# Optimization experiments

Measured on AMD Instinct MI355X. Metric: run time of the kernel, lower is better.

The kernel has to match this reference:

```python
import jax, jax.numpy as jnp
import numpy as np

B, C_IN, C_OUT, K, H, W = 8, 512, 512, 3, 32, 32
EPS = 1e-8


def _fir_filter():
    f1 = jnp.array([1.0, 3.0, 3.0, 1.0], dtype=jnp.float32)
    f = jnp.outer(f1, f1)
    f = f / f.sum()
    return f * 4.0  # gain = 2**2, filter.ndim/2 == 1


def setup_inputs() -> dict:
    key = jax.random.key(0)
    k1, k2, k3 = jax.random.split(key, 3)
    x = jax.random.normal(k1, (B, C_IN, H, W), dtype=jnp.float32)
    styles = jax.random.normal(k2, (B, C_IN), dtype=jnp.float32)
    w = jax.random.normal(k3, (C_OUT, C_IN, K, K), dtype=jnp.float32)  # lr_multiplier=1
    return {"x": x, "styles": styles, "w": w}


def reference(x, styles, w):
    batch = x.shape[0]
    gain = 1.0 / np.sqrt(C_OUT * C_IN * K * K)
    # modulate: [B, O, I, kh, kw]
    wm = (w[None] * gain) * (styles[:, None, :, None, None] + 1.0)
    # demodulate
    dcoefs = jax.lax.rsqrt(jnp.sum(wm * wm, axis=(2, 3, 4)) + EPS)  # [B, O]
    wm = wm * dcoefs[:, :, None, None, None]
    # fused modconv: batch folded into channels/groups
    x1 = x.reshape(1, batch * C_IN, H, W)
    # torch conv_transpose2d(stride=2, padding=0, groups=B) == dilated conv with
    # spatially flipped kernel, lhs_dilation=2, padding=K-1 on each side.
    w_eq = jnp.flip(wm, axis=(-2, -1)).reshape(batch * C_OUT, C_IN, K, K)
    y = jax.lax.conv_general_dilated(
        x1, w_eq,
        window_strides=(1, 1),
        padding=[(K - 1, K - 1), (K - 1, K - 1)],
        lhs_dilation=(2, 2),
        feature_group_count=batch,
        dimension_numbers=("NCHW", "OIHW", "NCHW"),
    )  # [1, B*O, 2H+1, 2W+1]
    # Upfirdn2d: up=1, down=1, pad=[1,1,1,1], depthwise 4x4 FIR (cross-correlation;
    # filter is symmetric so no flip needed)
    C = batch * C_OUT
    f = jnp.broadcast_to(_fir_filter()[None, None], (C, 1, 4, 4))
    y = jax.lax.conv_general_dilated(
        y, f,
        window_strides=(1, 1),
        padding=[(1, 1), (1, 1)],
        feature_group_count=C,
        dimension_numbers=("NCHW", "OIHW", "NCHW"),
    )  # [1, B*O, 2H, 2W]
    return y.reshape(batch, C_OUT, 2 * H, 2 * W)
```

## Files before the change

### kernel.cpp

```cpp
#include <hip/hip_runtime.h>
#include <stdint.h>


#define DI __device__ __forceinline__

typedef __bf16 bf16x8 __attribute__((ext_vector_type(8)));
typedef float f32x4 __attribute__((ext_vector_type(4)));

DI float bf2f(ushort u) { union { uint32_t i; float f; } v; v.i = ((uint32_t)u) << 16; return v.f; }
DI ushort f2bf(float f) {
  union { float f; uint32_t i; } v; v.f = f;
  uint32_t x = v.i;
  return (ushort)((x + 0x7FFFu + ((x >> 16) & 1u)) >> 16);
}

#define GAIN (1.0f / 1536.0f)

__global__ __launch_bounds__(256) void k_prep(const float* __restrict__ w,
                                              const float* __restrict__ styles,
                                              const float* __restrict__ x,
                                              ushort* __restrict__ Wm,
                                              ushort* __restrict__ xt) {
  __shared__ union {
    struct { float ss[4096]; float dc[8]; float wred[4][8]; } wp;
    float tl[32][257];
  } sm;
  const int t = threadIdx.x;
  if (blockIdx.x < 512) {
    const int o = blockIdx.x;
#pragma unroll
    for (int j = 0; j < 4; j++) {
      const int idx = (t + j * 256) * 4;
      *(float4*)&sm.wp.ss[idx] = *(const float4*)&styles[idx];
    }
    float wreg[18];
    const float* wp_ = w + o * 4608 + t * 18;
#pragma unroll
    for (int k = 0; k < 9; k++) {
      float2 v2 = *(const float2*)(wp_ + 2 * k);
      wreg[2 * k] = v2.x;
      wreg[2 * k + 1] = v2.y;
    }
    float q0 = 0.f, q1 = 0.f;
#pragma unroll
    for (int k = 0; k < 9; k++) {
      q0 += wreg[k] * wreg[k];
      q1 += wreg[9 + k] * wreg[9 + k];
    }
    __syncthreads();
    float pb[8];
#pragma unroll
    for (int b = 0; b < 8; b++) {
      float s0 = sm.wp.ss[b * 512 + 2 * t] + 1.0f;
      float s1 = sm.wp.ss[b * 512 + 2 * t + 1] + 1.0f;
      pb[b] = s0 * s0 * q0 + s1 * s1 * q1;
    }
#pragma unroll
    for (int b = 0; b < 8; b++)
#pragma unroll
      for (int off = 32; off > 0; off >>= 1) pb[b] += __shfl_down(pb[b], off, 64);
    const int wid = t >> 6, lane = t & 63;
    if (lane == 0) {
#pragma unroll
      for (int b = 0; b < 8; b++) sm.wp.wred[wid][b] = pb[b];
    }
    __syncthreads();
    if (t < 8)
      sm.wp.dc[t] = rsqrtf((sm.wp.wred[0][t] + sm.wp.wred[1][t] + sm.wp.wred[2][t] + sm.wp.wred[3][t]) *
                               (GAIN * GAIN) + 1e-8f);
    __syncthreads();
#pragma unroll
    for (int b = 0; b < 8; b++) {
      const float d = sm.wp.dc[b];
      const float s0 = GAIN * (sm.wp.ss[b * 512 + 2 * t] + 1.0f) * d;
      const float s1 = GAIN * (sm.wp.ss[b * 512 + 2 * t + 1] + 1.0f) * d;
      ushort* base = Wm + ((size_t)(b * 9) * 512 + o) * 512 + 2 * t;
#pragma unroll
      for (int tap = 0; tap < 9; tap++) {
        ushort2 val = make_ushort2(f2bf(wreg[tap] * s0), f2bf(wreg[9 + tap] * s1));
        *(ushort2*)(base + (size_t)tap * 262144) = val;
      }
    }
  } else {
    const int idx = blockIdx.x - 512;
    const int hw0 = (idx & 3) * 256, i0 = ((idx >> 2) & 15) * 32, b = idx >> 6;
    const float* xb = x + b * (512 * 1024);
#pragma unroll
    for (int p = 0; p < 8; p++) {
      const int r = p * 4 + (t >> 6);
      const int c4 = (t & 63) * 4;
      float4 v = *(const float4*)&xb[(i0 + r) * 1024 + hw0 + c4];
      sm.tl[r][c4] = v.x; sm.tl[r][c4 + 1] = v.y; sm.tl[r][c4 + 2] = v.z; sm.tl[r][c4 + 3] = v.w;
    }
    __syncthreads();
    ushort* xtb = xt + b * (1024 * 512);
#pragma unroll
    for (int p = 0; p < 8; p++) {
      const int hw = p * 32 + (t >> 3);
      const int i4 = (t & 7) * 4;
      ushort4 v = make_ushort4(f2bf(sm.tl[i4][hw]), f2bf(sm.tl[i4 + 1][hw]),
                               f2bf(sm.tl[i4 + 2][hw]), f2bf(sm.tl[i4 + 3][hw]));
      *(ushort4*)&xtb[(hw0 + hw) * 512 + i0 + i4] = v;
    }
  }
}

__global__ __launch_bounds__(512, 2) void k_gemm(const ushort* __restrict__ A,
                                                 const ushort* __restrict__ Bt,
                                                 ushort* __restrict__ C) {
  __shared__ __attribute__((aligned(128))) char smem[114688];
  const int id = blockIdx.x;
  const int batch = id & 7;
  const int rem = id >> 3;
  const int mt = rem >> 2, nt = rem & 3;
  const int m0 = mt * 192, n0 = nt * 256;
  const ushort* Ag = A + (size_t)batch * (4608 * 512);
  const ushort* Bg = Bt + (size_t)batch * (1024 * 512);
  ushort* Cg = C + (size_t)batch * (4608 * 1024);

  const int tid = threadIdx.x;
  const int w = tid >> 6, lane = tid & 63;
  const int wm = w >> 2, wn = w & 3;
  const int lq = lane >> 4, l15 = lane & 15, l7 = lane & 7;
  const int rlow = lane >> 3;
  const int ssw = (lane & 7) ^ rlow;

  const char* pA = (const char*)Ag + (size_t)(m0 + w * 24 + rlow) * 1024 + ssw * 16;
  const char* pB = (const char*)Bg + (size_t)(n0 + w * 32 + rlow) * 1024 + ssw * 16;
  char* dA = smem + w * 3072;
  char* dB = smem + 49152 + w * 4096;

#define GLL(srcp, dstp)                                                                     \
  __builtin_amdgcn_global_load_lds((const __attribute__((address_space(1))) void*)(srcp),   \
                                   (__attribute__((address_space(3))) void*)(dstp), 16, 0, 0)
#define STAGE_A(buf, kt)                                            \
  do {                                                              \
    GLL(pA + 0 * 8192 + (kt) * 128, dA + (buf) * 24576 + 0 * 1024); \
    GLL(pA + 1 * 8192 + (kt) * 128, dA + (buf) * 24576 + 1 * 1024); \
    GLL(pA + 2 * 8192 + (kt) * 128, dA + (buf) * 24576 + 2 * 1024); \
  } while (0)
#define STAGE_B(buf, kt)                                            \
  do {                                                              \
    GLL(pB + 0 * 8192 + (kt) * 128, dB + (buf) * 32768 + 0 * 1024); \
    GLL(pB + 1 * 8192 + (kt) * 128, dB + (buf) * 32768 + 1 * 1024); \
    GLL(pB + 2 * 8192 + (kt) * 128, dB + (buf) * 32768 + 2 * 1024); \
    GLL(pB + 3 * 8192 + (kt) * 128, dB + (buf) * 32768 + 3 * 1024); \
  } while (0)
#define CF asm volatile("" ::: "memory")
#define BAR()                          \
  do {                                 \
    CF;                                \
    __builtin_amdgcn_s_barrier();      \
    CF;                                \
  } while (0)

  const char* Ard = smem + (wm * 96 + l15) * 128;
  const char* Brd = smem + 49152 + (wn * 64 + l15) * 128;
  const int s0o = (lq ^ l7) * 16;
  const int s1o = ((4 + lq) ^ l7) * 16;

  f32x4 acc[6][4];
  const f32x4 z4 = {0.f, 0.f, 0.f, 0.f};
#pragma unroll
  for (int i = 0; i < 6; ++i)
#pragma unroll
    for (int n = 0; n < 4; ++n) acc[i][n] = z4;

  STAGE_A(0, 0); STAGE_B(0, 0);
  STAGE_A(1, 1); STAGE_B(1, 1);
  asm volatile("s_waitcnt vmcnt(7)" ::: "memory");
  BAR();

#pragma unroll
  for (int t = 0; t < 8; ++t) {
    const int buf = t & 1;
    const char* Ab = Ard + buf * 24576;
    const char* Bb = Brd + buf * 32768;
    bf16x8 a[3][2], a2[3][2], b[4][2];
#pragma unroll
    for (int i = 0; i < 3; ++i) {
      a[i][0] = *(const bf16x8*)(Ab + i * 2048 + s0o);
      a[i][1] = *(const bf16x8*)(Ab + i * 2048 + s1o);
    }
#pragma unroll
    for (int n = 0; n < 2; ++n) {
      b[n][0] = *(const bf16x8*)(Bb + n * 2048 + s0o);
      b[n][1] = *(const bf16x8*)(Bb + n * 2048 + s1o);
    }
    BAR();
    __builtin_amdgcn_s_setprio(1);
#pragma unroll
    for (int kk = 0; kk < 2; ++kk)
#pragma unroll
      for (int n = 0; n < 2; ++n)
#pragma unroll
        for (int i = 0; i < 3; ++i)
          acc[i][n] = __builtin_amdgcn_mfma_f32_16x16x32_bf16(a[i][kk], b[n][kk], acc[i][n], 0, 0, 0);
    __builtin_amdgcn_s_setprio(0);
    BAR();
#pragma unroll
    for (int n = 2; n < 4; ++n) {
      b[n][0] = *(const bf16x8*)(Bb + n * 2048 + s0o);
      b[n][1] = *(const bf16x8*)(Bb + n * 2048 + s1o);
    }
    BAR();
    __builtin_amdgcn_s_setprio(1);
#pragma unroll
    for (int kk = 0; kk < 2; ++kk)
#pragma unroll
      for (int n = 2; n < 4; ++n)
#pragma unroll
        for (int i = 0; i < 3; ++i)
          acc[i][n] = __builtin_amdgcn_mfma_f32_16x16x32_bf16(a[i][kk], b[n][kk], acc[i][n], 0, 0, 0);
    __builtin_amdgcn_s_setprio(0);
    BAR();
#pragma unroll
    for (int i = 0; i < 3; ++i) {
      a2[i][0] = *(const bf16x8*)(Ab + (3 + i) * 2048 + s0o);
      a2[i][1] = *(const bf16x8*)(Ab + (3 + i) * 2048 + s1o);
    }
    if (t < 6) STAGE_B(buf, t + 2);
    BAR();
    __builtin_amdgcn_s_setprio(1);
#pragma unroll
    for (int kk = 0; kk < 2; ++kk)
#pragma unroll
      for (int n = 0; n < 2; ++n)
#pragma unroll
        for (int i = 0; i < 3; ++i)
          acc[3 + i][n] = __builtin_amdgcn_mfma_f32_16x16x32_bf16(a2[i][kk], b[n][kk], acc[3 + i][n], 0, 0, 0);
    __builtin_amdgcn_s_setprio(0);
    BAR();
    if (t < 6) STAGE_A(buf, t + 2);
    __builtin_amdgcn_s_setprio(1);
#pragma unroll
    for (int kk = 0; kk < 2; ++kk)
#pragma unroll
      for (int n = 2; n < 4; ++n)
#pragma unroll
        for (int i = 0; i < 3; ++i)
          acc[3 + i][n] = __builtin_amdgcn_mfma_f32_16x16x32_bf16(a2[i][kk], b[n][kk], acc[3 + i][n], 0, 0, 0);
    __builtin_amdgcn_s_setprio(0);
    if (t < 6) {
      asm volatile("s_waitcnt vmcnt(7)" ::: "memory");
    } else if (t == 6) {
      asm volatile("s_waitcnt vmcnt(0)" ::: "memory");
    }
    BAR();
  }

  ushort* cs = (ushort*)smem;
#pragma unroll
  for (int p = 0; p < 2; ++p) {
    if (p) BAR();
    if (wm == p) {
#pragma unroll
      for (int mi = 0; mi < 6; ++mi)
#pragma unroll
        for (int n = 0; n < 4; ++n) {
          const int row = mi * 16 + lq * 4;
          const int col = wn * 64 + n * 16 + l15;
          const f32x4 v = acc[mi][n];
#pragma unroll
          for (int r = 0; r < 4; ++r) cs[(row + r) * 264 + col] = f2bf(v[r]);
        }
    }
    BAR();
#pragma unroll
    for (int j = 0; j < 6; ++j) {
      const int idx = j * 512 + tid;
      const int row = idx >> 5, c = idx & 31;
      *(uint4*)(Cg + (size_t)(m0 + p * 96 + row) * 1024 + n0 + c * 8) =
          *(const uint4*)(cs + row * 264 + c * 8);
    }
  }
#undef GLL
#undef STAGE_A
#undef STAGE_B
#undef CF
#undef BAR
}

__global__ __launch_bounds__(512) void k_fir(const ushort* __restrict__ C,
                                             float* __restrict__ out) {
  const int bo = blockIdx.x;
  const int b = bo >> 9, o = bo & 511;
  __shared__ __attribute__((aligned(16))) ushort Ct[9 * 1024];
  __shared__ float V[3 * 64 * 36];
  const ushort* Cb = C + ((size_t)(b * 9) * 512 + o) * 1024;
  for (int c = threadIdx.x; c < 1152; c += 512) {
    const int tap = c >> 7, off = (c & 127) * 8;
    *(uint4*)&Ct[tap * 1024 + off] = *(const uint4*)&Cb[(size_t)tap * 524288 + off];
  }
  __syncthreads();
#pragma unroll
  for (int j = 0; j < 3; j++) {
    const int gidx = threadIdx.x + j * 512;
    const int kw = gidx >> 9;
    const int rem = gidx & 511;
    const int u = rem >> 3;
    const int w0 = (rem & 7) * 4;
    float a0 = 0.f, a1 = 0.f, a2 = 0.f, a3 = 0.f;
#pragma unroll
    for (int kh = 0; kh < 3; kh++) {
      const int s0 = (kh + 1 + u) & 1;
#pragma unroll
      for (int d = 0; d < 2; d++) {
        const int h = (u + s0 + 2 * d - 1 - kh) >> 1;
        const bool ok = (h >= 0) & (h < 32);
        const float cf = ok ? ((s0 == d) ? 1.f : 3.f) : 0.f;
        const int hh = ok ? h : 0;
        const uint2 cv = *(const uint2*)&Ct[kh * 3072 + kw * 1024 + hh * 32 + w0];
        a0 += cf * bf2f((ushort)(cv.x & 0xffff));
        a1 += cf * bf2f((ushort)(cv.x >> 16));
        a2 += cf * bf2f((ushort)(cv.y & 0xffff));
        a3 += cf * bf2f((ushort)(cv.y >> 16));
      }
    }
    *(float4*)&V[kw * 2304 + u * 36 + w0] = make_float4(a0, a1, a2, a3);
  }
  __syncthreads();
  const size_t ob = (size_t)bo * 4096;
#pragma unroll
  for (int j = 0; j < 2; j++) {
    const int px4 = threadIdx.x + j * 512;
    const int u = px4 >> 4;
    const int v0 = (px4 & 15) * 4;
    float r[4] = {0.f, 0.f, 0.f, 0.f};
#pragma unroll
    for (int q = 0; q < 4; q++) {
      const int v = v0 + q;
#pragma unroll
      for (int kw = 0; kw < 3; kw++) {
        const int t0 = (kw + 1 + v) & 1;
#pragma unroll
        for (int d = 0; d < 2; d++) {
          const int wx = (v + t0 + 2 * d - 1 - kw) >> 1;
          const bool ok = (wx >= 0) & (wx < 32);
          const float cf = ok ? ((t0 == d) ? 1.f : 3.f) : 0.f;
          const int ww = ok ? wx : 0;
          r[q] += cf * V[kw * 2304 + u * 36 + ww];
        }
      }
      r[q] *= 0.0625f;
    }
    *(float4*)&out[ob + u * 64 + v0] = make_float4(r[0], r[1], r[2], r[3]);
  }
}

extern "C" void kernel_launch(void* const* d_in, const int* in_sizes, int n_in,
                              void* d_out, int out_size, void* d_ws, size_t ws_size,
                              hipStream_t stream) {
  (void)in_sizes; (void)n_in; (void)out_size; (void)ws_size;
  const float* x = (const float*)d_in[0];
  const float* styles = (const float*)d_in[1];
  const float* w = (const float*)d_in[2];
  float* out = (float*)d_out;
  char* ws = (char*)d_ws;
  ushort* Wm = (ushort*)ws;
  ushort* XT = (ushort*)(ws + 37748736);
  ushort* C = (ushort*)(ws + 37748736 + 8388608);

  k_prep<<<1024, 256, 0, stream>>>(w, styles, x, Wm, XT);
  k_gemm<<<768, 512, 0, stream>>>(Wm, XT, C);
  k_fir<<<4096, 512, 0, stream>>>(C, out);
}
```

Measured before the change: 157.0 us.

## Shrink GEMM tile to 128x256 with BK=32 for higher occupancy

The batched GEMM tile drops from 192x256 with BK=64 to 128x256 with BK=32. Shared memory falls from 112KB to 48KB and launch bounds allow four blocks per CU, with 1152 blocks instead of 768. The software pipeline is simplified to single-stage prefetch with a full vmcnt(0) wait and one barrier per k-step, replacing the interleaved split-phase schedule. Occupancy rises, but each tile reuses its operands less, barrier overhead per FLOP is higher, and the wait is less overlapped.

```diff
diff --git a/kernel.cpp b/kernel.cpp
--- a/kernel.cpp
+++ b/kernel.cpp
@@ -105,15 +105,15 @@
   }
 }
 
-__global__ __launch_bounds__(512, 2) void k_gemm(const ushort* __restrict__ A,
+__global__ __launch_bounds__(512, 4) void k_gemm(const ushort* __restrict__ A,
                                                  const ushort* __restrict__ Bt,
                                                  ushort* __restrict__ C) {
-  __shared__ __attribute__((aligned(128))) char smem[114688];
+  __shared__ __attribute__((aligned(128))) char smem[49152];
   const int id = blockIdx.x;
   const int batch = id & 7;
   const int rem = id >> 3;
   const int mt = rem >> 2, nt = rem & 3;
-  const int m0 = mt * 192, n0 = nt * 256;
+  const int m0 = mt * 128, n0 = nt * 256;
   const ushort* Ag = A + (size_t)batch * (4608 * 512);
   const ushort* Bg = Bt + (size_t)batch * (1024 * 512);
   ushort* Cg = C + (size_t)batch * (4608 * 1024);
@@ -121,30 +121,30 @@
   const int tid = threadIdx.x;
   const int w = tid >> 6, lane = tid & 63;
   const int wm = w >> 2, wn = w & 3;
-  const int lq = lane >> 4, l15 = lane & 15, l7 = lane & 7;
-  const int rlow = lane >> 3;
-  const int ssw = (lane & 7) ^ rlow;
-
-  const char* pA = (const char*)Ag + (size_t)(m0 + w * 24 + rlow) * 1024 + ssw * 16;
-  const char* pB = (const char*)Bg + (size_t)(n0 + w * 32 + rlow) * 1024 + ssw * 16;
-  char* dA = smem + w * 3072;
-  char* dB = smem + 49152 + w * 4096;
+  const int lq = lane >> 4, l15 = lane & 15;
+
+  const int srow = lane >> 2;
+  const int sslot = (lane & 3) ^ ((lane >> 3) & 3);
+  const char* gsrc[3];
+  int ldst[3];
+#pragma unroll
+  for (int q = 0; q < 3; ++q) {
+    const int idx = 3 * w + q;
+    const bool isA = idx < 8;
+    const int ch = isA ? idx : idx - 8;
+    const int grow = (isA ? m0 : n0) + ch * 16 + srow;
+    gsrc[q] = (const char*)(isA ? Ag : Bg) + (size_t)grow * 1024 + sslot * 16;
+    ldst[q] = (isA ? 0 : 8192) + ch * 1024;
+  }
 
 #define GLL(srcp, dstp)                                                                     \
   __builtin_amdgcn_global_load_lds((const __attribute__((address_space(1))) void*)(srcp),   \
                                    (__attribute__((address_space(3))) void*)(dstp), 16, 0, 0)
-#define STAGE_A(buf, kt)                                            \
+#define ISSUE(buf, kt)                                              \
   do {                                                              \
-    GLL(pA + 0 * 8192 + (kt) * 128, dA + (buf) * 24576 + 0 * 1024); \
-    GLL(pA + 1 * 8192 + (kt) * 128, dA + (buf) * 24576 + 1 * 1024); \
-    GLL(pA + 2 * 8192 + (kt) * 128, dA + (buf) * 24576 + 2 * 1024); \
-  } while (0)
-#define STAGE_B(buf, kt)                                            \
-  do {                                                              \
-    GLL(pB + 0 * 8192 + (kt) * 128, dB + (buf) * 32768 + 0 * 1024); \
-    GLL(pB + 1 * 8192 + (kt) * 128, dB + (buf) * 32768 + 1 * 1024); \
-    GLL(pB + 2 * 8192 + (kt) * 128, dB + (buf) * 32768 + 2 * 1024); \
-    GLL(pB + 3 * 8192 + (kt) * 128, dB + (buf) * 32768 + 3 * 1024); \
+    _Pragma("unroll")                                               \
+    for (int q = 0; q < 3; ++q)                                     \
+      GLL(gsrc[q] + (kt) * 64, smem + (buf) * 24576 + ldst[q]);     \
   } while (0)
 #define CF asm volatile("" ::: "memory")
 #define BAR()                          \
@@ -154,98 +154,38 @@
     CF;                                \
   } while (0)
 
-  const char* Ard = smem + (wm * 96 + l15) * 128;
-  const char* Brd = smem + 49152 + (wn * 64 + l15) * 128;
-  const int s0o = (lq ^ l7) * 16;
-  const int s1o = ((4 + lq) ^ l7) * 16;
-
-  f32x4 acc[6][4];
+  const int so = (lq ^ ((l15 >> 1) & 3)) * 16;
+  const char* Ard = smem + (wm * 64 + l15) * 64 + so;
+  const char* Brd = smem + 8192 + (wn * 64 + l15) * 64 + so;
+
+  f32x4 acc[4][4];
   const f32x4 z4 = {0.f, 0.f, 0.f, 0.f};
 #pragma unroll
-  for (int i = 0; i < 6; ++i)
+  for (int i = 0; i < 4; ++i)
 #pragma unroll
     for (int n = 0; n < 4; ++n) acc[i][n] = z4;
 
-  STAGE_A(0, 0); STAGE_B(0, 0);
-  STAGE_A(1, 1); STAGE_B(1, 1);
-  asm volatile("s_waitcnt vmcnt(7)" ::: "memory");
+  ISSUE(0, 0);
+  asm volatile("s_waitcnt vmcnt(0)" ::: "memory");
   BAR();
 
-#pragma unroll
-  for (int t = 0; t < 8; ++t) {
+#pragma unroll 2
+  for (int t = 0; t < 16; ++t) {
     const int buf = t & 1;
-    const char* Ab = Ard + buf * 24576;
-    const char* Bb = Brd + buf * 32768;
-    bf16x8 a[3][2], a2[3][2], b[4][2];
-#pragma unroll
-    for (int i = 0; i < 3; ++i) {
-      a[i][0] = *(const bf16x8*)(Ab + i * 2048 + s0o);
-      a[i][1] = *(const bf16x8*)(Ab + i * 2048 + s1o);
-    }
-#pragma unroll
-    for (int n = 0; n < 2; ++n) {
-      b[n][0] = *(const bf16x8*)(Bb + n * 2048 + s0o);
-      b[n][1] = *(const bf16x8*)(Bb + n * 2048 + s1o);
-    }
-    BAR();
+    if (t < 15) ISSUE(buf ^ 1, t + 1);
+    bf16x8 a[4], b[4];
+#pragma unroll
+    for (int i = 0; i < 4; ++i) a[i] = *(const bf16x8*)(Ard + buf * 24576 + i * 1024);
+#pragma unroll
+    for (int n = 0; n < 4; ++n) b[n] = *(const bf16x8*)(Brd + buf * 24576 + n * 1024);
     __builtin_amdgcn_s_setprio(1);
 #pragma unroll
-    for (int kk = 0; kk < 2; ++kk)
-#pragma unroll
-      for (int n = 0; n < 2; ++n)
-#pragma unroll
-        for (int i = 0; i < 3; ++i)
-          acc[i][n] = __builtin_amdgcn_mfma_f32_16x16x32_bf16(a[i][kk], b[n][kk], acc[i][n], 0, 0, 0);
+    for (int n = 0; n < 4; ++n)
+#pragma unroll
+      for (int i = 0; i < 4; ++i)
+        acc[i][n] = __builtin_amdgcn_mfma_f32_16x16x32_bf16(a[i], b[n], acc[i][n], 0, 0, 0);
     __builtin_amdgcn_s_setprio(0);
-    BAR();
-#pragma unroll
-    for (int n = 2; n < 4; ++n) {
-      b[n][0] = *(const bf16x8*)(Bb + n * 2048 + s0o);
-      b[n][1] = *(const bf16x8*)(Bb + n * 2048 + s1o);
-    }
-    BAR();
-    __builtin_amdgcn_s_setprio(1);
-#pragma unroll
-    for (int kk = 0; kk < 2; ++kk)
-#pragma unroll
-      for (int n = 2; n < 4; ++n)
-#pragma unroll
-        for (int i = 0; i < 3; ++i)
-          acc[i][n] = __builtin_amdgcn_mfma_f32_16x16x32_bf16(a[i][kk], b[n][kk], acc[i][n], 0, 0, 0);
-    __builtin_amdgcn_s_setprio(0);
-    BAR();
-#pragma unroll
-    for (int i = 0; i < 3; ++i) {
-      a2[i][0] = *(const bf16x8*)(Ab + (3 + i) * 2048 + s0o);
-      a2[i][1] = *(const bf16x8*)(Ab + (3 + i) * 2048 + s1o);
-    }
-    if (t < 6) STAGE_B(buf, t + 2);
-    BAR();
-    __builtin_amdgcn_s_setprio(1);
-#pragma unroll
-    for (int kk = 0; kk < 2; ++kk)
-#pragma unroll
-      for (int n = 0; n < 2; ++n)
-#pragma unroll
-        for (int i = 0; i < 3; ++i)
-          acc[3 + i][n] = __builtin_amdgcn_mfma_f32_16x16x32_bf16(a2[i][kk], b[n][kk], acc[3 + i][n], 0, 0, 0);
-    __builtin_amdgcn_s_setprio(0);
-    BAR();
-    if (t < 6) STAGE_A(buf, t + 2);
-    __builtin_amdgcn_s_setprio(1);
-#pragma unroll
-    for (int kk = 0; kk < 2; ++kk)
-#pragma unroll
-      for (int n = 2; n < 4; ++n)
-#pragma unroll
-        for (int i = 0; i < 3; ++i)
-          acc[3 + i][n] = __builtin_amdgcn_mfma_f32_16x16x32_bf16(a2[i][kk], b[n][kk], acc[3 + i][n], 0, 0, 0);
-    __builtin_amdgcn_s_setprio(0);
-    if (t < 6) {
-      asm volatile("s_waitcnt vmcnt(7)" ::: "memory");
-    } else if (t == 6) {
-      asm volatile("s_waitcnt vmcnt(0)" ::: "memory");
-    }
+    if (t < 15) asm volatile("s_waitcnt vmcnt(0)" ::: "memory");
     BAR();
   }
 
@@ -255,7 +195,7 @@
     if (p) BAR();
     if (wm == p) {
 #pragma unroll
-      for (int mi = 0; mi < 6; ++mi)
+      for (int mi = 0; mi < 4; ++mi)
 #pragma unroll
         for (int n = 0; n < 4; ++n) {
           const int row = mi * 16 + lq * 4;
@@ -267,16 +207,15 @@
     }
     BAR();
 #pragma unroll
-    for (int j = 0; j < 6; ++j) {
+    for (int j = 0; j < 4; ++j) {
       const int idx = j * 512 + tid;
       const int row = idx >> 5, c = idx & 31;
-      *(uint4*)(Cg + (size_t)(m0 + p * 96 + row) * 1024 + n0 + c * 8) =
+      *(uint4*)(Cg + (size_t)(m0 + p * 64 + row) * 1024 + n0 + c * 8) =
           *(const uint4*)(cs + row * 264 + c * 8);
     }
   }
 #undef GLL
-#undef STAGE_A
-#undef STAGE_B
+#undef ISSUE
 #undef CF
 #undef BAR
 }
@@ -362,6 +301,6 @@
   ushort* C = (ushort*)(ws + 37748736 + 8388608);
 
   k_prep<<<1024, 256, 0, stream>>>(w, styles, x, Wm, XT);
-  k_gemm<<<768, 512, 0, stream>>>(Wm, XT, C);
+  k_gemm<<<1152, 512, 0, stream>>>(Wm, XT, C);
   k_fir<<<4096, 512, 0, stream>>>(C, out);
 }
```

Measured after the change: 163.5 us. +4.1%, slower.

## Move style modulation onto activations and demod into GEMM epilogue, share weights

Applied to the files above, without the earlier changes.

Instead of building per-batch modulated bf16 weights (8x the weight tensor), the prep kernel writes one shared gain-scaled weight copy, scales the transposed activations by (style+1), and stores demodulation coefficients separately. The GEMM reads the shared weight matrix for every batch and multiplies each output row by its demod coefficient in the epilogue. This removes most of the prep write traffic and lets the GEMM reuse the same A tiles from L2 across batches. The cost is an extra per-element multiply in the epilogue and a small coefficient load, plus slightly different bf16 rounding.

```diff
diff --git a/kernel.cpp b/kernel.cpp
--- a/kernel.cpp
+++ b/kernel.cpp
@@ -19,12 +19,14 @@
 __global__ __launch_bounds__(256) void k_prep(const float* __restrict__ w,
                                               const float* __restrict__ styles,
                                               const float* __restrict__ x,
-                                              ushort* __restrict__ Wm,
-                                              ushort* __restrict__ xt) {
+                                              ushort* __restrict__ Wp,
+                                              float* __restrict__ dcg,
+                                              ushort* __restrict__ xs) {
   __shared__ union {
-    struct { float ss[4096]; float dc[8]; float wred[4][8]; } wp;
+    struct { float ss[4096]; float wred[4][8]; } wp;
     float tl[32][257];
   } sm;
+  __shared__ float sst[32];
   const int t = threadIdx.x;
   if (blockIdx.x < 512) {
     const int o = blockIdx.x;
@@ -41,6 +43,14 @@
       wreg[2 * k] = v2.x;
       wreg[2 * k + 1] = v2.y;
     }
+    {
+      ushort* base = Wp + (size_t)o * 512 + 2 * t;
+#pragma unroll
+      for (int tap = 0; tap < 9; tap++) {
+        ushort2 val = make_ushort2(f2bf(GAIN * wreg[tap]), f2bf(GAIN * wreg[9 + tap]));
+        *(ushort2*)(base + (size_t)tap * 262144) = val;
+      }
+    }
     float q0 = 0.f, q1 = 0.f;
 #pragma unroll
     for (int k = 0; k < 9; k++) {
@@ -66,25 +76,13 @@
     }
     __syncthreads();
     if (t < 8)
-      sm.wp.dc[t] = rsqrtf((sm.wp.wred[0][t] + sm.wp.wred[1][t] + sm.wp.wred[2][t] + sm.wp.wred[3][t]) *
-                               (GAIN * GAIN) + 1e-8f);
-    __syncthreads();
-#pragma unroll
-    for (int b = 0; b < 8; b++) {
-      const float d = sm.wp.dc[b];
-      const float s0 = GAIN * (sm.wp.ss[b * 512 + 2 * t] + 1.0f) * d;
-      const float s1 = GAIN * (sm.wp.ss[b * 512 + 2 * t + 1] + 1.0f) * d;
-      ushort* base = Wm + ((size_t)(b * 9) * 512 + o) * 512 + 2 * t;
-#pragma unroll
-      for (int tap = 0; tap < 9; tap++) {
-        ushort2 val = make_ushort2(f2bf(wreg[tap] * s0), f2bf(wreg[9 + tap] * s1));
-        *(ushort2*)(base + (size_t)tap * 262144) = val;
-      }
-    }
+      dcg[t * 512 + o] = rsqrtf((sm.wp.wred[0][t] + sm.wp.wred[1][t] + sm.wp.wred[2][t] +
+                                 sm.wp.wred[3][t]) * (GAIN * GAIN) + 1e-8f);
   } else {
     const int idx = blockIdx.x - 512;
     const int hw0 = (idx & 3) * 256, i0 = ((idx >> 2) & 15) * 32, b = idx >> 6;
     const float* xb = x + b * (512 * 1024);
+    if (t < 32) sst[t] = styles[b * 512 + i0 + t] + 1.0f;
 #pragma unroll
     for (int p = 0; p < 8; p++) {
       const int r = p * 4 + (t >> 6);
@@ -93,13 +91,15 @@
       sm.tl[r][c4] = v.x; sm.tl[r][c4 + 1] = v.y; sm.tl[r][c4 + 2] = v.z; sm.tl[r][c4 + 3] = v.w;
     }
     __syncthreads();
-    ushort* xtb = xt + b * (1024 * 512);
+    ushort* xtb = xs + b * (1024 * 512);
 #pragma unroll
     for (int p = 0; p < 8; p++) {
       const int hw = p * 32 + (t >> 3);
       const int i4 = (t & 7) * 4;
-      ushort4 v = make_ushort4(f2bf(sm.tl[i4][hw]), f2bf(sm.tl[i4 + 1][hw]),
-                               f2bf(sm.tl[i4 + 2][hw]), f2bf(sm.tl[i4 + 3][hw]));
+      ushort4 v = make_ushort4(f2bf(sm.tl[i4][hw] * sst[i4]),
+                               f2bf(sm.tl[i4 + 1][hw] * sst[i4 + 1]),
+                               f2bf(sm.tl[i4 + 2][hw] * sst[i4 + 2]),
+                               f2bf(sm.tl[i4 + 3][hw] * sst[i4 + 3]));
       *(ushort4*)&xtb[(hw0 + hw) * 512 + i0 + i4] = v;
     }
   }
@@ -107,14 +107,16 @@
 
 __global__ __launch_bounds__(512, 2) void k_gemm(const ushort* __restrict__ A,
                                                  const ushort* __restrict__ Bt,
+                                                 const float* __restrict__ dcoef,
                                                  ushort* __restrict__ C) {
   __shared__ __attribute__((aligned(128))) char smem[114688];
+  __shared__ float dcl[192];
   const int id = blockIdx.x;
   const int batch = id & 7;
   const int rem = id >> 3;
   const int mt = rem >> 2, nt = rem & 3;
   const int m0 = mt * 192, n0 = nt * 256;
-  const ushort* Ag = A + (size_t)batch * (4608 * 512);
+  const ushort* Ag = A;
   const ushort* Bg = Bt + (size_t)batch * (1024 * 512);
   ushort* Cg = C + (size_t)batch * (4608 * 1024);
 
@@ -124,6 +126,8 @@
   const int lq = lane >> 4, l15 = lane & 15, l7 = lane & 7;
   const int rlow = lane >> 3;
   const int ssw = (lane & 7) ^ rlow;
+
+  if (tid < 192) dcl[tid] = dcoef[batch * 512 + ((m0 + tid) & 511)];
 
   const char* pA = (const char*)Ag + (size_t)(m0 + w * 24 + rlow) * 1024 + ssw * 16;
   const char* pB = (const char*)Bg + (size_t)(n0 + w * 32 + rlow) * 1024 + ssw * 16;
@@ -262,7 +266,8 @@
           const int col = wn * 64 + n * 16 + l15;
           const f32x4 v = acc[mi][n];
 #pragma unroll
-          for (int r = 0; r < 4; ++r) cs[(row + r) * 264 + col] = f2bf(v[r]);
+          for (int r = 0; r < 4; ++r)
+            cs[(row + r) * 264 + col] = f2bf(v[r] * dcl[p * 96 + row + r]);
         }
     }
     BAR();
@@ -357,11 +362,12 @@
   const float* w = (const float*)d_in[2];
   float* out = (float*)d_out;
   char* ws = (char*)d_ws;
-  ushort* Wm = (ushort*)ws;
-  ushort* XT = (ushort*)(ws + 37748736);
-  ushort* C = (ushort*)(ws + 37748736 + 8388608);
-
-  k_prep<<<1024, 256, 0, stream>>>(w, styles, x, Wm, XT);
-  k_gemm<<<768, 512, 0, stream>>>(Wm, XT, C);
+  ushort* Wp = (ushort*)ws;
+  float* dcg = (float*)(ws + 4718592);
+  ushort* XS = (ushort*)(ws + 4734976);
+  ushort* C = (ushort*)(ws + 13123584);
+
+  k_prep<<<1024, 256, 0, stream>>>(w, styles, x, Wp, dcg, XS);
+  k_gemm<<<768, 512, 0, stream>>>(Wp, XS, dcg, C);
   k_fir<<<4096, 512, 0, stream>>>(C, out);
 }
```

Result: no change. 159.5 us (+1.6%).
